# Optimization experiments

Measured on AMD Instinct MI355X. Metric: run time of the kernel, lower is better.

Reference implementation:

```python
import jax, jax.numpy as jnp
import numpy as np

B, S, D = 4, 2048, 768
H, R = 12, 8
Dh = D // H


def setup_inputs() -> dict:
    key = jax.random.key(0)
    ks = jax.random.split(key, 12)
    s_in = 1.0 / np.sqrt(D)
    s_r = 1.0 / np.sqrt(R)
    return {
        "x": jax.random.normal(ks[0], (B, S, D), jnp.float32),
        "Wq0": jax.random.normal(ks[1], (D, D), jnp.float32) * s_in,
        "Aq": jax.random.normal(ks[2], (D, R), jnp.float32) * s_in,
        "Bq": jax.random.normal(ks[3], (R, D), jnp.float32) * s_r,
        "Wk0": jax.random.normal(ks[4], (D, D), jnp.float32) * s_in,
        "Ak": jax.random.normal(ks[5], (D, R), jnp.float32) * s_in,
        "Bk": jax.random.normal(ks[6], (R, D), jnp.float32) * s_r,
        "Wv0": jax.random.normal(ks[7], (D, D), jnp.float32) * s_in,
        "Av": jax.random.normal(ks[8], (D, R), jnp.float32) * s_in,
        "Bv": jax.random.normal(ks[9], (R, D), jnp.float32) * s_r,
        "Wo": jax.random.normal(ks[10], (D, D), jnp.float32) * s_in,
        "bo": jnp.zeros((D,), jnp.float32),
    }


def _lora(x, W0, A, Bm):
    # x @ W0 + (x @ A) @ B  -- low-rank adapter on frozen W0
    return x @ W0 + (x @ A) @ Bm


def _split_heads(t):
    # [B,S,D] -> [B,H,S,Dh]
    return t.reshape(B, S, H, Dh).transpose(0, 2, 1, 3)


def reference(x, Wq0, Aq, Bq, Wk0, Ak, Bk, Wv0, Av, Bv, Wo, bo):
    q = _split_heads(_lora(x, Wq0, Aq, Bq))
    k = _split_heads(_lora(x, Wk0, Ak, Bk))
    v = _split_heads(_lora(x, Wv0, Av, Bv))
    scale = 1.0 / jnp.sqrt(jnp.asarray(Dh, x.dtype))
    scores = jnp.einsum("bhqd,bhkd->bhqk", q, k) * scale  # [B,H,S,S]
    weights = jax.nn.softmax(scores, axis=-1)
    attn = jnp.einsum("bhqk,bhkd->bhqd", weights, v)
    concat = attn.transpose(0, 2, 1, 3).reshape(B, S, D)
    return concat @ Wo + bo
```

## Files before the change

kernel.cpp:

```cpp
#include <hip/hip_runtime.h>
#include <hip/hip_bf16.h>


typedef unsigned short ushort_t;
typedef __bf16 bf16x8 __attribute__((ext_vector_type(8)));
typedef float f32x4 __attribute__((ext_vector_type(4)));
typedef float f32x16 __attribute__((ext_vector_type(16)));
typedef unsigned short ushort8 __attribute__((ext_vector_type(8)));
typedef unsigned short ushort4_t __attribute__((ext_vector_type(4)));
typedef unsigned int uint4v __attribute__((ext_vector_type(4)));
typedef __attribute__((address_space(1))) unsigned int gu32;
typedef __attribute__((address_space(3))) unsigned int lu32;

__device__ __forceinline__ unsigned short f2bf(float f) {
  unsigned int u = __builtin_bit_cast(unsigned int, f);
  u += 0x7fffu + ((u >> 16) & 1u);
  return (unsigned short)(u >> 16);
}

__device__ __forceinline__ void gld_lds16(const void* g, void* s) {
  __builtin_amdgcn_global_load_lds((gu32*)(unsigned long long)g,
                                   (lu32*)(unsigned int)(unsigned long long)s,
                                   16, 0, 0);
}

__device__ __forceinline__ f32x4 mfma16(bf16x8 a, bf16x8 b, f32x4 c) {
  return __builtin_amdgcn_mfma_f32_16x16x32_bf16(a, b, c, 0, 0, 0);
}

__device__ __forceinline__ f32x16 mfma32(bf16x8 a, bf16x8 b, f32x16 c) {
  return __builtin_amdgcn_mfma_f32_32x32x16_bf16(a, b, c, 0, 0, 0);
}

__device__ __forceinline__ unsigned int cvtpk(float a, float b) {
  unsigned int r;
  asm("v_cvt_pk_bf16_f32 %0, %1, %2" : "=v"(r) : "v"(a), "v"(b));
  return r;
}

__global__ __launch_bounds__(256) void prep_weights(
    const float* __restrict__ Wq0, const float* __restrict__ Aq, const float* __restrict__ Bq,
    const float* __restrict__ Wk0, const float* __restrict__ Ak, const float* __restrict__ Bk,
    const float* __restrict__ Wv0, const float* __restrict__ Av, const float* __restrict__ Bv,
    const float* __restrict__ Wo,
    ushort_t* __restrict__ WeffT, ushort_t* __restrict__ WoT)
{
  __shared__ float tile[32][33];
  __shared__ float tA[32][8];
  __shared__ float tB[8][32];
  const int mat = blockIdx.y;
  const int kt = blockIdx.x / 24, nt = blockIdx.x % 24;
  const int k0 = kt * 32, n0 = nt * 32;
  const float* W0 = (mat == 0) ? Wq0 : (mat == 1) ? Wk0 : (mat == 2) ? Wv0 : Wo;
  const float* Am = (mat == 0) ? Aq : (mat == 1) ? Ak : (mat == 2) ? Av : nullptr;
  const float* Bm = (mat == 0) ? Bq : (mat == 1) ? Bk : (mat == 2) ? Bv : nullptr;
  const int tid = threadIdx.x;
#pragma unroll
  for (int i = 0; i < 4; i++) {
    int rr = i * 8 + (tid >> 5), c = tid & 31;
    tile[rr][c] = W0[(k0 + rr) * 768 + n0 + c];
  }
  if (Am) {
    tA[tid >> 3][tid & 7] = Am[(k0 + (tid >> 3)) * 8 + (tid & 7)];
    tB[tid >> 5][tid & 31] = Bm[(tid >> 5) * 768 + n0 + (tid & 31)];
  }
  __syncthreads();
#pragma unroll
  for (int i = 0; i < 4; i++) {
    int kk = tid & 31;
    int nn = i * 8 + (tid >> 5);
    float val = tile[kk][nn];
    if (Am) {
#pragma unroll
      for (int rr = 0; rr < 8; rr++) val += tA[kk][rr] * tB[rr][nn];
    }
    int n = n0 + nn, kg = k0 + kk;
    if (mat < 3) WeffT[((long)mat * 768 + n) * 768 + kg] = f2bf(val);
    else         WoT[(long)n * 768 + kg] = f2bf(val);
  }
}

__global__ __launch_bounds__(256) void cast_x(const float* __restrict__ x,
                                              ushort_t* __restrict__ xb)
{
  long i = (long)blockIdx.x * 256 + threadIdx.x;
  const float4* xp = (const float4*)x;
  float4 a = xp[i * 2], c = xp[i * 2 + 1];
  ushort8 rv;
  rv[0] = f2bf(a.x); rv[1] = f2bf(a.y); rv[2] = f2bf(a.z); rv[3] = f2bf(a.w);
  rv[4] = f2bf(c.x); rv[5] = f2bf(c.y); rv[6] = f2bf(c.z); rv[7] = f2bf(c.w);
  *(ushort8*)&xb[i * 8] = rv;
}

template <int MODE>
__global__ __launch_bounds__(256) void gemm_bt(
    const ushort_t* __restrict__ A, const ushort_t* __restrict__ Bt,
    ushort_t* __restrict__ q, ushort_t* __restrict__ kbuf, ushort_t* __restrict__ vt,
    float* __restrict__ out, const float* __restrict__ bo)
{
  constexpr int K = 768;
  __shared__ ushort_t As[128 * 64];
  __shared__ ushort_t Bs[128 * 64];
  const int tid = threadIdx.x;
  const int l = tid & 63, w = tid >> 6;
  const int wm = w >> 1, wn = w & 1;
  const int lr = l & 15, lg = l >> 4;
  const long rowBase = (long)blockIdx.x * 128;
  const long colBase = (long)blockIdx.y * 128;
  f32x4 acc[4][4] = {};

  for (int k0 = 0; k0 < K; k0 += 64) {
    __syncthreads();
#pragma unroll
    for (int i = 0; i < 4; i++) {
      int ci = i * 256 + tid;
      gld_lds16(A + (rowBase + (ci >> 3)) * K + k0 + (ci & 7) * 8, &As[ci * 8]);
    }
#pragma unroll
    for (int i = 0; i < 4; i++) {
      int ci = i * 256 + tid;
      gld_lds16(Bt + (colBase + (ci >> 3)) * K + k0 + (ci & 7) * 8, &Bs[ci * 8]);
    }
    asm volatile("s_waitcnt vmcnt(0)" ::: "memory");
    __syncthreads();
#pragma unroll
    for (int ks = 0; ks < 2; ks++) {
      bf16x8 af[4], bf[4];
#pragma unroll
      for (int m = 0; m < 4; m++)
        af[m] = *(const bf16x8*)&As[(wm * 64 + m * 16 + lr) * 64 + ks * 32 + lg * 8];
#pragma unroll
      for (int n = 0; n < 4; n++)
        bf[n] = *(const bf16x8*)&Bs[(wn * 64 + n * 16 + lr) * 64 + ks * 32 + lg * 8];
#pragma unroll
      for (int m = 0; m < 4; m++)
#pragma unroll
        for (int n = 0; n < 4; n++)
          acc[m][n] = mfma16(af[m], bf[n], acc[m][n]);
    }
  }

  if (MODE == 0) {
    const int mat = (int)(colBase / 768);
    if (mat == 2) {
      const long cb = colBase - 1536;
#pragma unroll
      for (int m = 0; m < 4; m++) {
        long srow = rowBase + wm * 64 + m * 16 + lg * 4;
        long b = srow >> 11, s = srow & 2047;
        long sp = (s & ~12L) | ((s & 4) << 1) | ((s & 8) >> 1);
#pragma unroll
        for (int n = 0; n < 4; n++) {
          long col = cb + wn * 64 + n * 16 + lr;
          ushort4_t pk;
#pragma unroll
          for (int r = 0; r < 4; r++) pk[r] = f2bf(acc[m][n][r]);
          *(ushort4_t*)&vt[(b * 768 + col) * 2048 + sp] = pk;
        }
      }
    } else {
      ushort_t* dst = (mat == 0) ? q : kbuf;
      const float scl = (mat == 0) ? 0.125f * 1.4426950408889634f : 1.0f;
      const long cb = colBase - (long)mat * 768;
#pragma unroll
      for (int m = 0; m < 4; m++)
#pragma unroll
        for (int n = 0; n < 4; n++) {
          long col = cb + wn * 64 + n * 16 + lr;
#pragma unroll
          for (int r = 0; r < 4; r++) {
            long row = rowBase + wm * 64 + m * 16 + lg * 4 + r;
            dst[row * 768 + col] = f2bf(acc[m][n][r] * scl);
          }
        }
    }
  } else {
#pragma unroll
    for (int m = 0; m < 4; m++)
#pragma unroll
      for (int n = 0; n < 4; n++) {
        long col = colBase + wn * 64 + n * 16 + lr;
        float bv = bo[col];
#pragma unroll
        for (int r = 0; r < 4; r++) {
          long row = rowBase + wm * 64 + m * 16 + lg * 4 + r;
          out[row * 768 + col] = acc[m][n][r] + bv;
        }
      }
  }
}

__global__ __launch_bounds__(256) void attn_fwd(
    const ushort_t* __restrict__ Q, const ushort_t* __restrict__ Kg,
    const ushort_t* __restrict__ VtG, ushort_t* __restrict__ O)
{
  constexpr int D = 768, S = 2048;
  __shared__ ushort_t Ks[2][64 * 64];
  __shared__ ushort_t Vs[2][64 * 64];
  const int tid = threadIdx.x;
  const int l = tid & 63, w = tid >> 6;
  const int q32 = l & 31, hi = l >> 5;
  const int i = blockIdx.x;
  const int xcd = i & 7, j = i >> 3;
  const int bh = xcd * 6 + (j >> 4);
  const int q0 = (j & 15) * 128;
  const int b = bh / 12, h = bh % 12;
  const ushort_t* Qb = Q + (long)b * S * D + h * 64;
  const ushort_t* Kb = Kg + (long)b * S * D + h * 64;
  const ushort_t* Vb = VtG + ((long)b * 768 + h * 64) * S;

  bf16x8 qf[4];
  {
    const ushort_t* qrow = Qb + (long)(q0 + w * 32 + q32) * D + hi * 8;
#pragma unroll
    for (int ks = 0; ks < 4; ks++) qf[ks] = *(const bf16x8*)&qrow[ks * 16];
  }

  int koff[2], voff[2];
#pragma unroll
  for (int it = 0; it < 2; it++) {
    int ci = it * 256 + tid, r = ci >> 3, c = ci & 7;
    koff[it] = r * D + ((c ^ (r & 7)) * 8);
    voff[it] = r * S + ((c ^ (r & 7)) * 8);
  }
  const int swz = q32 & 7;
  int rdoff[4];
#pragma unroll
  for (int ks = 0; ks < 4; ks++) rdoff[ks] = ((ks * 2 + hi) ^ swz) * 8;

  bf16x8 ones;
#pragma unroll
  for (int e = 0; e < 8; e++) ones[e] = (__bf16)1.0f;

  f32x16 oA = {}, oB = {}, osum = {};

  auto STAGE = [&](int kt, int bi) {
    const ushort_t* kp = Kb + (long)kt * 64 * D;
    const ushort_t* vp = Vb + kt * 64;
#pragma unroll
    for (int it = 0; it < 2; it++)
      gld_lds16(kp + koff[it], &Ks[bi][(it * 256 + tid) * 8]);
#pragma unroll
    for (int it = 0; it < 2; it++)
      gld_lds16(vp + voff[it], &Vs[bi][(it * 256 + tid) * 8]);
  };

  STAGE(0, 0);

  for (int kt = 0; kt < 32; kt++) {
    const int cur = kt & 1;
    STAGE((kt + 1) & 31, cur ^ 1);
    asm volatile("s_waitcnt vmcnt(4)" ::: "memory");
    __builtin_amdgcn_s_barrier();

    const ushort_t* ksb = &Ks[cur][0];
    const ushort_t* vsb = &Vs[cur][0];

    f32x16 s0 = {}, s1 = {};
    __builtin_amdgcn_s_setprio(1);
#pragma unroll
    for (int ks = 0; ks < 4; ks++) {
      bf16x8 kf0 = *(const bf16x8*)&ksb[q32 * 64 + rdoff[ks]];
      bf16x8 kf1 = *(const bf16x8*)&ksb[(32 + q32) * 64 + rdoff[ks]];
      s0 = mfma32(kf0, qf[ks], s0);
      s1 = mfma32(kf1, qf[ks], s1);
    }
    __builtin_amdgcn_s_setprio(0);

    unsigned int pw[16];
#pragma unroll
    for (int u = 0; u < 8; u++) {
      float a0 = __builtin_amdgcn_exp2f(s0[2 * u]);
      float a1 = __builtin_amdgcn_exp2f(s0[2 * u + 1]);
      pw[u] = cvtpk(a0, a1);
    }
#pragma unroll
    for (int u = 0; u < 8; u++) {
      float a0 = __builtin_amdgcn_exp2f(s1[2 * u]);
      float a1 = __builtin_amdgcn_exp2f(s1[2 * u + 1]);
      pw[8 + u] = cvtpk(a0, a1);
    }

    __builtin_amdgcn_s_setprio(1);
#pragma unroll
    for (int ks = 0; ks < 4; ks++) {
      uint4v w4 = {pw[4 * ks], pw[4 * ks + 1], pw[4 * ks + 2], pw[4 * ks + 3]};
      bf16x8 pa = __builtin_bit_cast(bf16x8, w4);
      bf16x8 vf0 = *(const bf16x8*)&vsb[q32 * 64 + rdoff[ks]];
      bf16x8 vf1 = *(const bf16x8*)&vsb[(32 + q32) * 64 + rdoff[ks]];
      oA = mfma32(pa, vf0, oA);
      oB = mfma32(pa, vf1, oB);
      osum = mfma32(pa, ones, osum);
    }
    __builtin_amdgcn_s_setprio(0);

    asm volatile("" ::: "memory");
    __builtin_amdgcn_s_barrier();
  }

#pragma unroll
  for (int reg = 0; reg < 16; reg++) {
    int row = (reg & 3) + 8 * (reg >> 2) + 4 * hi;
    float inv = 1.0f / osum[reg];
    long base = ((long)b * S + q0 + w * 32 + row) * D + h * 64 + q32;
    O[base] = f2bf(oA[reg] * inv);
    O[base + 32] = f2bf(oB[reg] * inv);
  }
}

extern "C" void kernel_launch(void* const* d_in, const int* in_sizes, int n_in,
                              void* d_out, int out_size, void* d_ws, size_t ws_size,
                              hipStream_t stream)
{
  const float* x   = (const float*)d_in[0];
  const float* Wq0 = (const float*)d_in[1];
  const float* Aq  = (const float*)d_in[2];
  const float* Bq  = (const float*)d_in[3];
  const float* Wk0 = (const float*)d_in[4];
  const float* Ak  = (const float*)d_in[5];
  const float* Bk  = (const float*)d_in[6];
  const float* Wv0 = (const float*)d_in[7];
  const float* Av  = (const float*)d_in[8];
  const float* Bv  = (const float*)d_in[9];
  const float* Wo  = (const float*)d_in[10];
  const float* bo  = (const float*)d_in[11];
  float* out = (float*)d_out;

  char* ws = (char*)d_ws;
  const long SZ = 8192L * 768 * 2;
  ushort_t* xb    = (ushort_t*)(ws);
  ushort_t* Qb    = (ushort_t*)(ws + SZ);
  ushort_t* Kb    = (ushort_t*)(ws + 2 * SZ);
  ushort_t* Vt    = (ushort_t*)(ws + 3 * SZ);
  ushort_t* At    = (ushort_t*)(ws + 4 * SZ);
  ushort_t* WeffT = (ushort_t*)(ws + 5 * SZ);
  ushort_t* WoT   = (ushort_t*)(ws + 5 * SZ + 2304L * 768 * 2);

  hipLaunchKernelGGL(prep_weights, dim3(576, 4), dim3(256), 0, stream,
                     Wq0, Aq, Bq, Wk0, Ak, Bk, Wv0, Av, Bv, Wo, WeffT, WoT);
  hipLaunchKernelGGL(cast_x, dim3(3072), dim3(256), 0, stream, x, xb);
  hipLaunchKernelGGL((gemm_bt<0>), dim3(64, 18), dim3(256), 0, stream,
                     xb, WeffT, Qb, Kb, Vt, (float*)nullptr, (const float*)nullptr);
  hipLaunchKernelGGL(attn_fwd, dim3(768), dim3(256), 0, stream, Qb, Kb, Vt, At);
  hipLaunchKernelGGL((gemm_bt<1>), dim3(64, 6), dim3(256), 0, stream,
                     At, WoT, (ushort_t*)nullptr, (ushort_t*)nullptr, (ushort_t*)nullptr,
                     out, bo);
}
```

Before: 174.8 us.

## Stage GEMM epilogue through LDS, triple-buffer attention K/V, drop row-sum MFMA

New measurement: 177.0 us. About the same (+1.2%).

```diff
diff --git a/kernel.cpp b/kernel.cpp
--- a/kernel.cpp
+++ b/kernel.cpp
@@ -99,8 +99,8 @@
     float* __restrict__ out, const float* __restrict__ bo)
 {
   constexpr int K = 768;
-  __shared__ ushort_t As[128 * 64];
-  __shared__ ushort_t Bs[128 * 64];
+  __shared__ __align__(16) ushort_t As[128 * 64];
+  __shared__ __align__(16) ushort_t Bs[128 * 64];
   const int tid = threadIdx.x;
   const int l = tid & 63, w = tid >> 6;
   const int wm = w >> 1, wn = w & 1;
@@ -142,21 +142,33 @@
 
   if (MODE == 0) {
     const int mat = (int)(colBase / 768);
+    __syncthreads();
+    ushort_t* myscr = (w < 2) ? &As[w * 4096] : &Bs[(w - 2) * 4096];
     if (mat == 2) {
       const long cb = colBase - 1536;
 #pragma unroll
       for (int m = 0; m < 4; m++) {
-        long srow = rowBase + wm * 64 + m * 16 + lg * 4;
-        long b = srow >> 11, s = srow & 2047;
-        long sp = (s & ~12L) | ((s & 4) << 1) | ((s & 8) >> 1);
+        int sp0 = m * 16 + ((lg & 1) << 3) + ((lg >> 1) << 2);
 #pragma unroll
         for (int n = 0; n < 4; n++) {
-          long col = cb + wn * 64 + n * 16 + lr;
+          int lcol = n * 16 + lr;
+          int ch = (sp0 >> 3) ^ (lcol & 7);
           ushort4_t pk;
 #pragma unroll
           for (int r = 0; r < 4; r++) pk[r] = f2bf(acc[m][n][r]);
-          *(ushort4_t*)&vt[(b * 768 + col) * 2048 + sp] = pk;
+          *(ushort4_t*)&myscr[lcol * 64 + ch * 8 + (sp0 & 7)] = pk;
         }
+      }
+      asm volatile("s_waitcnt lgkmcnt(0)" ::: "memory");
+      const long sB = rowBase + wm * 64;
+      const long bI = sB >> 11, sL = sB & 2047;
+      const long cg = cb + wn * 64;
+#pragma unroll
+      for (int it = 0; it < 8; it++) {
+        int cl = (l >> 3) + it * 8;
+        int ch = (l & 7) ^ (cl & 7);
+        ushort8 vv = *(const ushort8*)&myscr[cl * 64 + ch * 8];
+        *(ushort8*)&vt[(bI * 768 + cg + cl) * 2048 + sL + (l & 7) * 8] = vv;
       }
     } else {
       ushort_t* dst = (mat == 0) ? q : kbuf;
@@ -165,14 +177,22 @@
 #pragma unroll
       for (int m = 0; m < 4; m++)
 #pragma unroll
-        for (int n = 0; n < 4; n++) {
-          long col = cb + wn * 64 + n * 16 + lr;
+        for (int n = 0; n < 4; n++)
 #pragma unroll
           for (int r = 0; r < 4; r++) {
-            long row = rowBase + wm * 64 + m * 16 + lg * 4 + r;
-            dst[row * 768 + col] = f2bf(acc[m][n][r] * scl);
+            int lrow = m * 16 + lg * 4 + r, lcol = n * 16 + lr;
+            int ch = (lcol >> 3) ^ (lrow & 7);
+            myscr[lrow * 64 + ch * 8 + (lcol & 7)] = f2bf(acc[m][n][r] * scl);
           }
-        }
+      asm volatile("s_waitcnt lgkmcnt(0)" ::: "memory");
+      const long cg = cb + wn * 64;
+#pragma unroll
+      for (int it = 0; it < 8; it++) {
+        int rl = (l >> 3) + it * 8;
+        int ch = (l & 7) ^ (rl & 7);
+        ushort8 vv = *(const ushort8*)&myscr[rl * 64 + ch * 8];
+        *(ushort8*)&dst[(rowBase + wm * 64 + rl) * 768 + cg + (l & 7) * 8] = vv;
+      }
     }
   } else {
 #pragma unroll
@@ -195,8 +215,9 @@
     const ushort_t* __restrict__ VtG, ushort_t* __restrict__ O)
 {
   constexpr int D = 768, S = 2048;
-  __shared__ ushort_t Ks[2][64 * 64];
-  __shared__ ushort_t Vs[2][64 * 64];
+  __shared__ __align__(16) ushort_t Ks[3][64 * 64];
+  __shared__ __align__(16) ushort_t Vs[3][64 * 64];
+  __shared__ float Lrow[4][32];
   const int tid = threadIdx.x;
   const int l = tid & 63, w = tid >> 6;
   const int q32 = l & 31, hi = l >> 5;
@@ -228,11 +249,8 @@
 #pragma unroll
   for (int ks = 0; ks < 4; ks++) rdoff[ks] = ((ks * 2 + hi) ^ swz) * 8;
 
-  bf16x8 ones;
-#pragma unroll
-  for (int e = 0; e < 8; e++) ones[e] = (__bf16)1.0f;
-
-  f32x16 oA = {}, oB = {}, osum = {};
+  f32x16 oA = {}, oB = {};
+  float psum = 0.f;
 
   auto STAGE = [&](int kt, int bi) {
     const ushort_t* kp = Kb + (long)kt * 64 * D;
@@ -246,10 +264,11 @@
   };
 
   STAGE(0, 0);
+  int cur = 0;
 
   for (int kt = 0; kt < 32; kt++) {
-    const int cur = kt & 1;
-    STAGE((kt + 1) & 31, cur ^ 1);
+    int nxt = cur + 1; if (nxt == 3) nxt = 0;
+    STAGE((kt + 1) & 31, nxt);
     asm volatile("s_waitcnt vmcnt(4)" ::: "memory");
     __builtin_amdgcn_s_barrier();
 
@@ -272,12 +291,14 @@
     for (int u = 0; u < 8; u++) {
       float a0 = __builtin_amdgcn_exp2f(s0[2 * u]);
       float a1 = __builtin_amdgcn_exp2f(s0[2 * u + 1]);
+      psum += a0 + a1;
       pw[u] = cvtpk(a0, a1);
     }
 #pragma unroll
     for (int u = 0; u < 8; u++) {
       float a0 = __builtin_amdgcn_exp2f(s1[2 * u]);
       float a1 = __builtin_amdgcn_exp2f(s1[2 * u + 1]);
+      psum += a0 + a1;
       pw[8 + u] = cvtpk(a0, a1);
     }
 
@@ -290,18 +311,20 @@
       bf16x8 vf1 = *(const bf16x8*)&vsb[(32 + q32) * 64 + rdoff[ks]];
       oA = mfma32(pa, vf0, oA);
       oB = mfma32(pa, vf1, oB);
-      osum = mfma32(pa, ones, osum);
     }
     __builtin_amdgcn_s_setprio(0);
 
-    asm volatile("" ::: "memory");
-    __builtin_amdgcn_s_barrier();
-  }
+    cur = nxt;
+  }
+
+  float tot = psum + __shfl_xor(psum, 32, 64);
+  Lrow[w][q32] = tot;
+  asm volatile("s_waitcnt lgkmcnt(0)" ::: "memory");
 
 #pragma unroll
   for (int reg = 0; reg < 16; reg++) {
     int row = (reg & 3) + 8 * (reg >> 2) + 4 * hi;
-    float inv = 1.0f / osum[reg];
+    float inv = 1.0f / Lrow[w][row];
     long base = ((long)b * S + q0 + w * 32 + row) * D + h * 64 + q32;
     O[base] = f2bf(oA[reg] * inv);
     O[base + 32] = f2bf(oB[reg] * inv);
```
